# Optimization experiments

Hardware: AMD Instinct MI355X
Metric: run time of the kernel (lower is better)

## Reference

```python
import jax, jax.numpy as jnp
import numpy as np

D_K = 64  # per-head dim used for the 1/sqrt(d_k) scaling


def setup_inputs() -> dict:
    key = jax.random.key(0)
    k1, k2, k3, k4 = jax.random.split(key, 4)
    B, H, Lq, NB, NT, D = 4, 8, 512, 32, 128, 64
    q = jax.random.normal(k1, (B, H, Lq, D), dtype=jnp.float32)
    k = jax.random.normal(k2, (B, NB, H, NT, D), dtype=jnp.float32)
    v = jax.random.normal(k3, (B, NB, H, NT, D), dtype=jnp.float32)
    attn_s = jax.random.uniform(k4, (B, H, Lq, NB), dtype=jnp.float32)
    return {"q": q, "k": k, "v": v, "attn_s": attn_s}


def reference(q, k, v, attn_s):
    # q: [B,H,Lq,D]; k,v: [B,NB,H,NT,D]; attn_s: [B,H,Lq,NB]
    B, NB, H, NT, D = k.shape
    Lq = q.shape[2]
    scale = 1.0 / jnp.sqrt(jnp.asarray(D_K, dtype=q.dtype))
    # block-wise QK scores: [B,NB,H,Lq,NT] (q broadcast over blocks instead of expand+matmul)
    attn = jnp.einsum('bhqd,bnhtd->bnhqt', q * scale, k)
    weights = jax.nn.softmax(attn, axis=-1)            # per-block softmax over tokens
    attn_w = jnp.transpose(weights, (0, 2, 3, 1, 4))    # [B,H,Lq,NB,NT]
    attn_w = attn_w * attn_s[..., None]                 # sentence-level reweighting
    attn_w = attn_w.reshape(B, H, Lq, NB * NT)          # concat blocks (dropout p=0 -> identity)
    v_w = jnp.transpose(v, (0, 2, 1, 3, 4)).reshape(B, H, NB * NT, D)
    out = jnp.matmul(attn_w, v_w)                       # [B,H,Lq,D]
    out = jnp.transpose(out, (0, 2, 1, 3)).reshape(B, Lq, H * D)
    return out, attn_w
```

## Files before the change

kernel.cpp:

```cpp
#include <hip/hip_runtime.h>
#include <stdint.h>

constexpr int CB=4, CH=8, CLQ=512, CNB=32, CNT=128, CD=64;
constexpr int QT=16;
constexpr int PSTR=36;
constexpr int OSTR=68;

typedef __attribute__((ext_vector_type(8))) short short8;
typedef __attribute__((ext_vector_type(4))) float f32x4;

union Frag { uint32_t u[4]; short8 s8; };

__device__ inline uint32_t fb(float x){ union{float f;uint32_t u;} v; v.f=x; return v.u; }
__device__ inline float uf(uint32_t u){ union{float f;uint32_t u;} v; v.u=u; return v.f; }
__device__ inline uint32_t packhi(float a, float b){
    return (fb(b) & 0xffff0000u) | (fb(a) >> 16);
}

__device__ inline f32x4 mfma_bf16(const Frag& a, const Frag& b, f32x4 c){
    return __builtin_amdgcn_mfma_f32_16x16x32_bf16(a.s8, b.s8, c, 0, 0, 0);
}

__global__ __launch_bounds__(256, 4)
void sdpa_mfma_kernel(const float* __restrict__ qg, const float* __restrict__ kg,
                      const float* __restrict__ vg, const float* __restrict__ sg,
                      float* __restrict__ outg, float* __restrict__ awg)
{
    __shared__ float pbuf[4 * QT * PSTR];
    __shared__ float sums[2][64];
    __shared__ float as_t[CNB * QT];
    __shared__ float obuf[4 * QT * OSTR];

    const int tid  = threadIdx.x;
    const int wave = tid >> 6;
    const int lane = tid & 63;
    const int l15  = lane & 15;
    const int q8   = lane >> 4;

    const int bid = blockIdx.x;
    const int qt  = bid & 31;
    const int bh  = bid >> 5;
    const int b   = bh >> 3;
    const int h   = bh & 7;
    const int q0  = qt * QT;

    {
        const float* sbase = sg + ((size_t)bh * CLQ + q0) * CNB;
        #pragma unroll
        for (int e = 0; e < 2; ++e) {
            int idx = tid + e * 256;
            int r = idx >> 5, n = idx & 31;
            as_t[n * QT + r] = sbase[r * CNB + n];
        }
    }

    Frag qhi[2], qlo[2];
    {
        const float* qrow = qg + ((size_t)bh * CLQ + q0 + l15) * CD;
        #pragma unroll
        for (int s = 0; s < 2; ++s) {
            f32x4 a = *(const f32x4*)&qrow[s*32 + q8*8];
            f32x4 c = *(const f32x4*)&qrow[s*32 + q8*8 + 4];
            float e[8] = {a[0]*0.125f, a[1]*0.125f, a[2]*0.125f, a[3]*0.125f,
                          c[0]*0.125f, c[1]*0.125f, c[2]*0.125f, c[3]*0.125f};
            #pragma unroll
            for (int p = 0; p < 4; ++p) {
                float e0 = e[2*p], e1 = e[2*p+1];
                qhi[s].u[p] = packhi(e0, e1);
                float h0 = uf(fb(e0) & 0xffff0000u);
                float h1 = uf(fb(e1) & 0xffff0000u);
                qlo[s].u[p] = packhi(e0 - h0, e1 - h1);
            }
        }
    }

    f32x4 O[4];
    #pragma unroll
    for (int cd = 0; cd < 4; ++cd) O[cd] = (f32x4){0.f,0.f,0.f,0.f};

    float* pw = &pbuf[wave * QT * PSTR];

    for (int n = 0; n < CNB; ++n) {
        const float* kb = kg + ((size_t)((b*CNB + n)*CH + h)) * CNT * CD;
        const float* vb = vg + ((size_t)((b*CNB + n)*CH + h)) * CNT * CD + wave*32*CD;

        f32x4 S[2];
        #pragma unroll
        for (int c = 0; c < 2; ++c) {
            const float* kr = kb + (size_t)(wave*32 + c*16 + l15) * CD;
            Frag khi[2], klo[2];
            #pragma unroll
            for (int s = 0; s < 2; ++s) {
                f32x4 a = *(const f32x4*)&kr[s*32 + q8*8];
                f32x4 d = *(const f32x4*)&kr[s*32 + q8*8 + 4];
                float e[8] = {a[0],a[1],a[2],a[3],d[0],d[1],d[2],d[3]};
                #pragma unroll
                for (int p = 0; p < 4; ++p) {
                    float e0 = e[2*p], e1 = e[2*p+1];
                    khi[s].u[p] = packhi(e0, e1);
                    float h0 = uf(fb(e0) & 0xffff0000u);
                    float h1 = uf(fb(e1) & 0xffff0000u);
                    klo[s].u[p] = packhi(e0 - h0, e1 - h1);
                }
            }
            f32x4 acc = (f32x4){0.f,0.f,0.f,0.f};
            acc = mfma_bf16(qhi[0], khi[0], acc);
            acc = mfma_bf16(qhi[1], khi[1], acc);
            acc = mfma_bf16(qlo[0], khi[0], acc);
            acc = mfma_bf16(qlo[1], khi[1], acc);
            acc = mfma_bf16(qhi[0], klo[0], acc);
            acc = mfma_bf16(qhi[1], klo[1], acc);
            S[c] = acc;
        }

        float E0[4], E1[4], ps[4];
        #pragma unroll
        for (int r = 0; r < 4; ++r) {
            E0[r] = __expf(S[0][r]);
            E1[r] = __expf(S[1][r]);
            ps[r] = E0[r] + E1[r];
        }
        #pragma unroll
        for (int off = 1; off <= 8; off <<= 1) {
            #pragma unroll
            for (int r = 0; r < 4; ++r) ps[r] += __shfl_xor(ps[r], off, 64);
        }
        if (l15 == 0) {
            f32x4 t = {ps[0], ps[1], ps[2], ps[3]};
            *(f32x4*)&sums[n & 1][wave*16 + q8*4] = t;
        }
        __syncthreads();

        f32x4 d4 = (f32x4){0.f,0.f,0.f,0.f};
        #pragma unroll
        for (int wv = 0; wv < 4; ++wv)
            d4 += *(const f32x4*)&sums[n & 1][wv*16 + q8*4];
        const f32x4 asv = *(const f32x4*)&as_t[n*QT + q8*4];

        float fac[4];
        #pragma unroll
        for (int r = 0; r < 4; ++r) fac[r] = asv[r] / d4[r];

        #pragma unroll
        for (int r = 0; r < 4; ++r) {
            pw[(q8*4 + r)*PSTR + l15]      = E0[r] * fac[r];
            pw[(q8*4 + r)*PSTR + 16 + l15] = E1[r] * fac[r];
        }

        #pragma unroll
        for (int i = 0; i < 2; ++i) {
            int idx = lane + i*64;
            int row = idx >> 3, c4 = idx & 7;
            f32x4 pv = *(const f32x4*)&pw[row*PSTR + c4*4];
            *(f32x4*)&awg[(((size_t)bh*CLQ + q0 + row)*CNB + n)*CNT + wave*32 + c4*4] = pv;
        }

        Frag phi;
        {
            f32x4 a = *(const f32x4*)&pw[l15*PSTR + q8*8];
            f32x4 c = *(const f32x4*)&pw[l15*PSTR + q8*8 + 4];
            float e[8] = {a[0],a[1],a[2],a[3],c[0],c[1],c[2],c[3]};
            #pragma unroll
            for (int p = 0; p < 4; ++p) phi.u[p] = packhi(e[2*p], e[2*p+1]);
        }

        #pragma unroll
        for (int cd = 0; cd < 4; ++cd) {
            float vf[8];
            #pragma unroll
            for (int j = 0; j < 8; ++j)
                vf[j] = vb[(q8*8 + j)*CD + cd*16 + l15];
            Frag vh;
            #pragma unroll
            for (int p = 0; p < 4; ++p) vh.u[p] = packhi(vf[2*p], vf[2*p+1]);
            O[cd] = mfma_bf16(phi, vh, O[cd]);
        }
    }

    {
        float* ow = &obuf[wave * QT * OSTR];
        #pragma unroll
        for (int cd = 0; cd < 4; ++cd)
            #pragma unroll
            for (int r = 0; r < 4; ++r)
                ow[(q8*4 + r)*OSTR + cd*16 + l15] = O[cd][r];
    }
    __syncthreads();
    {
        int r = tid >> 4, dq = tid & 15;
        f32x4 acc = (f32x4){0.f,0.f,0.f,0.f};
        #pragma unroll
        for (int wv = 0; wv < 4; ++wv)
            acc += *(const f32x4*)&obuf[wv*QT*OSTR + r*OSTR + dq*4];
        *(f32x4*)&outg[((size_t)b*CLQ + q0 + r)*(CH*CD) + h*CD + dq*4] = acc;
    }
}

extern "C" void kernel_launch(void* const* d_in, const int* in_sizes, int n_in,
                              void* d_out, int out_size, void* d_ws, size_t ws_size,
                              hipStream_t stream) {
    const float* q = (const float*)d_in[0];
    const float* k = (const float*)d_in[1];
    const float* v = (const float*)d_in[2];
    const float* s = (const float*)d_in[3];
    float* out = (float*)d_out;
    float* aw  = out + (size_t)CB * CLQ * CH * CD;

    const int grid = CB * CH * (CLQ / QT);
    sdpa_mfma_kernel<<<grid, 256, 0, stream>>>(q, k, v, s, out, aw);
}
```

Baseline: 488.9 us.

## Precompute bf16 hi/lo K and transposed bf16 V in a prep kernel

A new prep kernel converts K into bf16 hi/lo split arrays and V into a transposed bf16 layout in workspace, once per call. The attention kernel then loads ready-made MFMA fragments with 128-bit loads instead of converting fp32 K/V in every block. It also reassigns work so each wave handles 8 whole blocks, which removes the per-block cross-wave sum reduction and its __syncthreads, and remaps block ids to group the heads. This costs an extra kernel launch plus workspace traffic. If the workspace is too small, the launcher falls back to the original kernel.

```diff
diff --git a/kernel.cpp b/kernel.cpp
--- a/kernel.cpp
+++ b/kernel.cpp
@@ -2,61 +2,102 @@
 #include <stdint.h>
 
 constexpr int CB=4, CH=8, CLQ=512, CNB=32, CNT=128, CD=64;
-constexpr int QT=16;
-constexpr int PSTR=36;
-constexpr int OSTR=68;
+constexpr size_t KVELEMS = (size_t)CB*CNB*CH*CNT*CD;
+constexpr size_t WS_NEED = KVELEMS * 2 * 3;
 
 typedef __attribute__((ext_vector_type(8))) short short8;
 typedef __attribute__((ext_vector_type(4))) float f32x4;
 
-union Frag { uint32_t u[4]; short8 s8; };
+union Frag { uint32_t u[4]; short8 s8; uint4 v; };
 
 __device__ inline uint32_t fb(float x){ union{float f;uint32_t u;} v; v.f=x; return v.u; }
 __device__ inline float uf(uint32_t u){ union{float f;uint32_t u;} v; v.u=u; return v.f; }
-__device__ inline uint32_t packhi(float a, float b){
-    return (fb(b) & 0xffff0000u) | (fb(a) >> 16);
-}
-
+__device__ inline uint32_t packhi(float a, float b){ return (fb(b)&0xffff0000u)|(fb(a)>>16); }
+__device__ inline uint32_t lopack(float a, float b){
+    float ra = a - uf(fb(a)&0xffff0000u);
+    float rb = b - uf(fb(b)&0xffff0000u);
+    return packhi(ra, rb);
+}
 __device__ inline f32x4 mfma_bf16(const Frag& a, const Frag& b, f32x4 c){
     return __builtin_amdgcn_mfma_f32_16x16x32_bf16(a.s8, b.s8, c, 0, 0, 0);
 }
 
+__global__ __launch_bounds__(256, 2)
+void prep_kernel(const float* __restrict__ kg, const float* __restrict__ vg,
+                 ushort* __restrict__ khi, ushort* __restrict__ klo, ushort* __restrict__ vt)
+{
+    __shared__ float vtile[64 * 132];
+    const int tid = threadIdx.x;
+    const size_t base = (size_t)blockIdx.x * (CNT*CD);
+
+    const float4* kb4 = (const float4*)(kg + base);
+    uint2* kh2 = (uint2*)(khi + base);
+    uint2* kl2 = (uint2*)(klo + base);
+    #pragma unroll
+    for (int j = 0; j < 8; ++j) {
+        int i4 = j*256 + tid;
+        float4 f = kb4[i4];
+        kh2[i4] = make_uint2(packhi(f.x,f.y), packhi(f.z,f.w));
+        kl2[i4] = make_uint2(lopack(f.x,f.y), lopack(f.z,f.w));
+    }
+
+    const float4* vb4 = (const float4*)(vg + base);
+    #pragma unroll
+    for (int it = 0; it < 8; ++it) {
+        int flat = it*256 + tid;
+        int t = flat >> 4, dg = flat & 15;
+        float4 f = vb4[t*16 + dg];
+        vtile[(dg*4+0)*132 + t] = f.x;
+        vtile[(dg*4+1)*132 + t] = f.y;
+        vtile[(dg*4+2)*132 + t] = f.z;
+        vtile[(dg*4+3)*132 + t] = f.w;
+    }
+    __syncthreads();
+
+    {
+        int d = tid >> 2, tq = tid & 3;
+        float fv[32];
+        #pragma unroll
+        for (int c = 0; c < 8; ++c) {
+            f32x4 r = *(const f32x4*)&vtile[d*132 + tq*32 + c*4];
+            fv[c*4+0]=r[0]; fv[c*4+1]=r[1]; fv[c*4+2]=r[2]; fv[c*4+3]=r[3];
+        }
+        uint4* dst = (uint4*)(vt + base + d*CNT + tq*32);
+        #pragma unroll
+        for (int j = 0; j < 4; ++j) {
+            uint4 o;
+            o.x = packhi(fv[j*8+0], fv[j*8+1]);
+            o.y = packhi(fv[j*8+2], fv[j*8+3]);
+            o.z = packhi(fv[j*8+4], fv[j*8+5]);
+            o.w = packhi(fv[j*8+6], fv[j*8+7]);
+            dst[j] = o;
+        }
+    }
+}
+
 __global__ __launch_bounds__(256, 4)
-void sdpa_mfma_kernel(const float* __restrict__ qg, const float* __restrict__ kg,
-                      const float* __restrict__ vg, const float* __restrict__ sg,
-                      float* __restrict__ outg, float* __restrict__ awg)
+void attn_kernel(const float* __restrict__ qg, const ushort* __restrict__ khig,
+                 const ushort* __restrict__ klog, const ushort* __restrict__ vtg,
+                 const float* __restrict__ sg, float* __restrict__ outg,
+                 float* __restrict__ awg)
 {
-    __shared__ float pbuf[4 * QT * PSTR];
-    __shared__ float sums[2][64];
-    __shared__ float as_t[CNB * QT];
-    __shared__ float obuf[4 * QT * OSTR];
+    __shared__ float pbuf[4][16*36];
+    __shared__ float obuf[4][16*68];
 
     const int tid  = threadIdx.x;
-    const int wave = tid >> 6;
-    const int lane = tid & 63;
-    const int l15  = lane & 15;
-    const int q8   = lane >> 4;
+    const int wave = tid >> 6, lane = tid & 63;
+    const int l15  = lane & 15, q8 = lane >> 4;
 
     const int bid = blockIdx.x;
-    const int qt  = bid & 31;
-    const int bh  = bid >> 5;
-    const int b   = bh >> 3;
-    const int h   = bh & 7;
-    const int q0  = qt * QT;
-
-    {
-        const float* sbase = sg + ((size_t)bh * CLQ + q0) * CNB;
-        #pragma unroll
-        for (int e = 0; e < 2; ++e) {
-            int idx = tid + e * 256;
-            int r = idx >> 5, n = idx & 31;
-            as_t[n * QT + r] = sbase[r * CNB + n];
-        }
-    }
+    const int kk  = bid >> 3;
+    const int bh  = (bid & 7)*4 + (kk & 3);
+    const int qt  = kk >> 2;
+    const int b   = bh >> 3, h = bh & 7;
+    const int q0  = qt * 16;
 
     Frag qhi[2], qlo[2];
     {
-        const float* qrow = qg + ((size_t)bh * CLQ + q0 + l15) * CD;
+        const float* qrow = qg + ((size_t)bh*CLQ + q0 + l15)*CD;
         #pragma unroll
         for (int s = 0; s < 2; ++s) {
             f32x4 a = *(const f32x4*)&qrow[s*32 + q8*8];
@@ -65,11 +106,8 @@
                           c[0]*0.125f, c[1]*0.125f, c[2]*0.125f, c[3]*0.125f};
             #pragma unroll
             for (int p = 0; p < 4; ++p) {
-                float e0 = e[2*p], e1 = e[2*p+1];
-                qhi[s].u[p] = packhi(e0, e1);
-                float h0 = uf(fb(e0) & 0xffff0000u);
-                float h1 = uf(fb(e1) & 0xffff0000u);
-                qlo[s].u[p] = packhi(e0 - h0, e1 - h1);
+                qhi[s].u[p] = packhi(e[2*p], e[2*p+1]);
+                qlo[s].u[p] = lopack(e[2*p], e[2*p+1]);
             }
         }
     }
@@ -78,17 +116,153 @@
     #pragma unroll
     for (int cd = 0; cd < 4; ++cd) O[cd] = (f32x4){0.f,0.f,0.f,0.f};
 
-    float* pw = &pbuf[wave * QT * PSTR];
+    float* pw = pbuf[wave];
+    const int n0 = wave * 8;
+
+    for (int nn = 0; nn < 8; ++nn) {
+        const int n = n0 + nn;
+        const size_t sb = (size_t)((b*CNB + n)*CH + h) * (CNT*CD);
+        const ushort* kh = khig + sb;
+        const ushort* kl = klog + sb;
+        const ushort* vb = vtg  + sb;
+
+        f32x4 E[8];
+        #pragma unroll
+        for (int c = 0; c < 8; ++c) {
+            const ushort* kr = kh + (c*16 + l15)*CD + q8*8;
+            const ushort* lr = kl + (c*16 + l15)*CD + q8*8;
+            Frag kh0, kh1, kl0, kl1;
+            kh0.v = *(const uint4*)(kr);
+            kh1.v = *(const uint4*)(kr + 32);
+            kl0.v = *(const uint4*)(lr);
+            kl1.v = *(const uint4*)(lr + 32);
+            f32x4 accA = (f32x4){0.f,0.f,0.f,0.f};
+            f32x4 accB = (f32x4){0.f,0.f,0.f,0.f};
+            accA = mfma_bf16(qhi[0], kh0, accA);
+            accB = mfma_bf16(qlo[0], kh0, accB);
+            accA = mfma_bf16(qhi[1], kh1, accA);
+            accB = mfma_bf16(qlo[1], kh1, accB);
+            accA = mfma_bf16(qhi[0], kl0, accA);
+            accB = mfma_bf16(qhi[1], kl1, accB);
+            E[c] = accA + accB;
+        }
+
+        float ps[4] = {0.f,0.f,0.f,0.f};
+        #pragma unroll
+        for (int c = 0; c < 8; ++c) {
+            #pragma unroll
+            for (int r = 0; r < 4; ++r) { E[c][r] = __expf(E[c][r]); ps[r] += E[c][r]; }
+        }
+        #pragma unroll
+        for (int off = 1; off <= 8; off <<= 1) {
+            #pragma unroll
+            for (int r = 0; r < 4; ++r) ps[r] += __shfl_xor(ps[r], off, 64);
+        }
+        float fac[4];
+        const float* srow = sg + ((size_t)bh*CLQ + q0 + q8*4)*CNB + n;
+        #pragma unroll
+        for (int r = 0; r < 4; ++r) fac[r] = srow[r*CNB] / ps[r];
+
+        #pragma unroll
+        for (int kc = 0; kc < 4; ++kc) {
+            #pragma unroll
+            for (int r = 0; r < 4; ++r) {
+                float p0 = E[kc*2][r]   * fac[r];
+                float p1 = E[kc*2+1][r] * fac[r];
+                pw[(q8*4+r)*36 + l15]      = p0;
+                pw[(q8*4+r)*36 + 16 + l15] = p1;
+                float* ab = awg + (((size_t)bh*CLQ + q0 + q8*4 + r)*CNB + n)*CNT + kc*32 + l15;
+                ab[0]  = p0;
+                ab[16] = p1;
+            }
+            Frag pf;
+            {
+                f32x4 a = *(const f32x4*)&pw[l15*36 + q8*8];
+                f32x4 c = *(const f32x4*)&pw[l15*36 + q8*8 + 4];
+                pf.u[0] = packhi(a[0],a[1]); pf.u[1] = packhi(a[2],a[3]);
+                pf.u[2] = packhi(c[0],c[1]); pf.u[3] = packhi(c[2],c[3]);
+            }
+            #pragma unroll
+            for (int cd = 0; cd < 4; ++cd) {
+                Frag vf;
+                vf.v = *(const uint4*)&vb[(cd*16 + l15)*CNT + kc*32 + q8*8];
+                O[cd] = mfma_bf16(pf, vf, O[cd]);
+            }
+        }
+    }
+
+    {
+        float* ow = obuf[wave];
+        #pragma unroll
+        for (int cd = 0; cd < 4; ++cd)
+            #pragma unroll
+            for (int r = 0; r < 4; ++r)
+                ow[(q8*4 + r)*68 + cd*16 + l15] = O[cd][r];
+    }
+    __syncthreads();
+    {
+        int r = tid >> 4, dq = tid & 15;
+        f32x4 acc = (f32x4){0.f,0.f,0.f,0.f};
+        #pragma unroll
+        for (int wv = 0; wv < 4; ++wv)
+            acc += *(const f32x4*)&obuf[wv][r*68 + dq*4];
+        *(f32x4*)&outg[((size_t)b*CLQ + q0 + r)*(CH*CD) + h*CD + dq*4] = acc;
+    }
+}
+
+constexpr int PSTR=36, OSTR=68;
+__global__ __launch_bounds__(256, 4)
+void sdpa_fallback_kernel(const float* __restrict__ qg, const float* __restrict__ kg,
+                          const float* __restrict__ vg, const float* __restrict__ sg,
+                          float* __restrict__ outg, float* __restrict__ awg)
+{
+    __shared__ float pbuf[4 * 16 * PSTR];
+    __shared__ float sums[2][64];
+    __shared__ float as_t[CNB * 16];
+    __shared__ float obuf[4 * 16 * OSTR];
+
+    const int tid = threadIdx.x, wave = tid>>6, lane = tid&63;
+    const int l15 = lane&15, q8 = lane>>4;
+    const int bid = blockIdx.x, qt = bid&31, bh = bid>>5, b = bh>>3, h = bh&7;
+    const int q0 = qt*16;
+
+    {
+        const float* sbase = sg + ((size_t)bh*CLQ + q0)*CNB;
+        #pragma unroll
+        for (int e = 0; e < 2; ++e) {
+            int idx = tid + e*256; int r = idx>>5, n = idx&31;
+            as_t[n*16 + r] = sbase[r*CNB + n];
+        }
+    }
+    Frag qhi[2], qlo[2];
+    {
+        const float* qrow = qg + ((size_t)bh*CLQ + q0 + l15)*CD;
+        #pragma unroll
+        for (int s = 0; s < 2; ++s) {
+            f32x4 a = *(const f32x4*)&qrow[s*32 + q8*8];
+            f32x4 c = *(const f32x4*)&qrow[s*32 + q8*8 + 4];
+            float e[8] = {a[0]*0.125f,a[1]*0.125f,a[2]*0.125f,a[3]*0.125f,
+                          c[0]*0.125f,c[1]*0.125f,c[2]*0.125f,c[3]*0.125f};
+            #pragma unroll
+            for (int p = 0; p < 4; ++p) {
+                qhi[s].u[p] = packhi(e[2*p], e[2*p+1]);
+                qlo[s].u[p] = lopack(e[2*p], e[2*p+1]);
+            }
+        }
+    }
+    f32x4 O[4];
+    #pragma unroll
+    for (int cd = 0; cd < 4; ++cd) O[cd] = (f32x4){0.f,0.f,0.f,0.f};
+    float* pw = &pbuf[wave * 16 * PSTR];
 
     for (int n = 0; n < CNB; ++n) {
-        const float* kb = kg + ((size_t)((b*CNB + n)*CH + h)) * CNT * CD;
-        const float* vb = vg + ((size_t)((b*CNB + n)*CH + h)) * CNT * CD + wave*32*CD;
-
+        const float* kb = kg + ((size_t)((b*CNB + n)*CH + h))*CNT*CD;
+        const float* vb = vg + ((size_t)((b*CNB + n)*CH + h))*CNT*CD + wave*32*CD;
         f32x4 S[2];
         #pragma unroll
         for (int c = 0; c < 2; ++c) {
-            const float* kr = kb + (size_t)(wave*32 + c*16 + l15) * CD;
-            Frag khi[2], klo[2];
+            const float* kr = kb + (size_t)(wave*32 + c*16 + l15)*CD;
+            Frag khA[2], klA[2];
             #pragma unroll
             for (int s = 0; s < 2; ++s) {
                 f32x4 a = *(const f32x4*)&kr[s*32 + q8*8];
@@ -96,89 +270,66 @@
                 float e[8] = {a[0],a[1],a[2],a[3],d[0],d[1],d[2],d[3]};
                 #pragma unroll
                 for (int p = 0; p < 4; ++p) {
-                    float e0 = e[2*p], e1 = e[2*p+1];
-                    khi[s].u[p] = packhi(e0, e1);
-                    float h0 = uf(fb(e0) & 0xffff0000u);
-                    float h1 = uf(fb(e1) & 0xffff0000u);
-                    klo[s].u[p] = packhi(e0 - h0, e1 - h1);
+                    khA[s].u[p] = packhi(e[2*p], e[2*p+1]);
+                    klA[s].u[p] = lopack(e[2*p], e[2*p+1]);
                 }
             }
             f32x4 acc = (f32x4){0.f,0.f,0.f,0.f};
-            acc = mfma_bf16(qhi[0], khi[0], acc);
-            acc = mfma_bf16(qhi[1], khi[1], acc);
-            acc = mfma_bf16(qlo[0], khi[0], acc);
-            acc = mfma_bf16(qlo[1], khi[1], acc);
-            acc = mfma_bf16(qhi[0], klo[0], acc);
-            acc = mfma_bf16(qhi[1], klo[1], acc);
+            acc = mfma_bf16(qhi[0], khA[0], acc);
+            acc = mfma_bf16(qhi[1], khA[1], acc);
+            acc = mfma_bf16(qlo[0], khA[0], acc);
+            acc = mfma_bf16(qlo[1], khA[1], acc);
+            acc = mfma_bf16(qhi[0], klA[0], acc);
+            acc = mfma_bf16(qhi[1], klA[1], acc);
             S[c] = acc;
         }
-
         float E0[4], E1[4], ps[4];
         #pragma unroll
+        for (int r = 0; r < 4; ++r) { E0[r]=__expf(S[0][r]); E1[r]=__expf(S[1][r]); ps[r]=E0[r]+E1[r]; }
+        #pragma unroll
+        for (int off = 1; off <= 8; off <<= 1)
+            #pragma unroll
+            for (int r = 0; r < 4; ++r) ps[r] += __shfl_xor(ps[r], off, 64);
+        if (l15 == 0) { f32x4 t = {ps[0],ps[1],ps[2],ps[3]}; *(f32x4*)&sums[n&1][wave*16 + q8*4] = t; }
+        __syncthreads();
+        f32x4 d4 = (f32x4){0.f,0.f,0.f,0.f};
+        #pragma unroll
+        for (int wv = 0; wv < 4; ++wv) d4 += *(const f32x4*)&sums[n&1][wv*16 + q8*4];
+        const f32x4 asv = *(const f32x4*)&as_t[n*16 + q8*4];
+        float fac[4];
+        #pragma unroll
+        for (int r = 0; r < 4; ++r) fac[r] = asv[r] / d4[r];
+        #pragma unroll
         for (int r = 0; r < 4; ++r) {
-            E0[r] = __expf(S[0][r]);
-            E1[r] = __expf(S[1][r]);
-            ps[r] = E0[r] + E1[r];
-        }
-        #pragma unroll
-        for (int off = 1; off <= 8; off <<= 1) {
-            #pragma unroll
-            for (int r = 0; r < 4; ++r) ps[r] += __shfl_xor(ps[r], off, 64);
-        }
-        if (l15 == 0) {
-            f32x4 t = {ps[0], ps[1], ps[2], ps[3]};
-            *(f32x4*)&sums[n & 1][wave*16 + q8*4] = t;
-        }
-        __syncthreads();
-
-        f32x4 d4 = (f32x4){0.f,0.f,0.f,0.f};
-        #pragma unroll
-        for (int wv = 0; wv < 4; ++wv)
-            d4 += *(const f32x4*)&sums[n & 1][wv*16 + q8*4];
-        const f32x4 asv = *(const f32x4*)&as_t[n*QT + q8*4];
-
-        float fac[4];
-        #pragma unroll
-        for (int r = 0; r < 4; ++r) fac[r] = asv[r] / d4[r];
-
-        #pragma unroll
-        for (int r = 0; r < 4; ++r) {
-            pw[(q8*4 + r)*PSTR + l15]      = E0[r] * fac[r];
-            pw[(q8*4 + r)*PSTR + 16 + l15] = E1[r] * fac[r];
-        }
-
+            pw[(q8*4+r)*PSTR + l15]      = E0[r]*fac[r];
+            pw[(q8*4+r)*PSTR + 16 + l15] = E1[r]*fac[r];
+        }
         #pragma unroll
         for (int i = 0; i < 2; ++i) {
-            int idx = lane + i*64;
-            int row = idx >> 3, c4 = idx & 7;
+            int idx = lane + i*64; int row = idx>>3, c4 = idx&7;
             f32x4 pv = *(const f32x4*)&pw[row*PSTR + c4*4];
             *(f32x4*)&awg[(((size_t)bh*CLQ + q0 + row)*CNB + n)*CNT + wave*32 + c4*4] = pv;
         }
-
         Frag phi;
         {
             f32x4 a = *(const f32x4*)&pw[l15*PSTR + q8*8];
             f32x4 c = *(const f32x4*)&pw[l15*PSTR + q8*8 + 4];
-            float e[8] = {a[0],a[1],a[2],a[3],c[0],c[1],c[2],c[3]};
-            #pragma unroll
-            for (int p = 0; p < 4; ++p) phi.u[p] = packhi(e[2*p], e[2*p+1]);
-        }
-
+            phi.u[0]=packhi(a[0],a[1]); phi.u[1]=packhi(a[2],a[3]);
+            phi.u[2]=packhi(c[0],c[1]); phi.u[3]=packhi(c[2],c[3]);
+        }
         #pragma unroll
         for (int cd = 0; cd < 4; ++cd) {
             float vf[8];
             #pragma unroll
-            for (int j = 0; j < 8; ++j)
-                vf[j] = vb[(q8*8 + j)*CD + cd*16 + l15];
+            for (int j = 0; j < 8; ++j) vf[j] = vb[(q8*8 + j)*CD + cd*16 + l15];
             Frag vh;
             #pragma unroll
             for (int p = 0; p < 4; ++p) vh.u[p] = packhi(vf[2*p], vf[2*p+1]);
             O[cd] = mfma_bf16(phi, vh, O[cd]);
         }
     }
-
-    {
-        float* ow = &obuf[wave * QT * OSTR];
+    {
+        float* ow = &obuf[wave * 16 * OSTR];
         #pragma unroll
         for (int cd = 0; cd < 4; ++cd)
             #pragma unroll
@@ -190,8 +341,7 @@
         int r = tid >> 4, dq = tid & 15;
         f32x4 acc = (f32x4){0.f,0.f,0.f,0.f};
         #pragma unroll
-        for (int wv = 0; wv < 4; ++wv)
-            acc += *(const f32x4*)&obuf[wv*QT*OSTR + r*OSTR + dq*4];
+        for (int wv = 0; wv < 4; ++wv) acc += *(const f32x4*)&obuf[wv*16*OSTR + r*OSTR + dq*4];
         *(f32x4*)&outg[((size_t)b*CLQ + q0 + r)*(CH*CD) + h*CD + dq*4] = acc;
     }
 }
@@ -206,6 +356,13 @@
     float* out = (float*)d_out;
     float* aw  = out + (size_t)CB * CLQ * CH * CD;
 
-    const int grid = CB * CH * (CLQ / QT);
-    sdpa_mfma_kernel<<<grid, 256, 0, stream>>>(q, k, v, s, out, aw);
-}
+    if (ws_size >= WS_NEED) {
+        ushort* khi = (ushort*)d_ws;
+        ushort* klo = khi + KVELEMS;
+        ushort* vt  = klo + KVELEMS;
+        prep_kernel<<<CB*CNB*CH, 256, 0, stream>>>(k, v, khi, klo, vt);
+        attn_kernel<<<1024, 256, 0, stream>>>(q, khi, klo, vt, s, out, aw);
+    } else {
+        sdpa_fallback_kernel<<<1024, 256, 0, stream>>>(q, k, v, s, out, aw);
+    }
+}
```

New measurement: 499.3 us. 2.1% more time.
